# Kernel optimization log

Measured on AMD Instinct MI355X. Metric: run time of the kernel, lower is better.

## Reference

```python
import jax, jax.numpy as jnp
import numpy as np

G = 512        # graphs in batch
N_PER = 256    # nodes per graph (equal-size graphs)
D = 128        # embed_dim
E_PER = 4096   # edges per graph
KEEP = 0.5
K = int(np.ceil(KEEP * N_PER))  # 128 nodes kept per graph (PyG topk: ceil(ratio*n))
N = G * N_PER
E = G * E_PER


def setup_inputs() -> dict:
    key = jax.random.key(0)
    k1, k2, k3, k4, k5 = jax.random.split(key, 5)
    x = jax.random.normal(k1, (N, D), jnp.float32)
    offs = (jnp.arange(G, dtype=jnp.int32) * N_PER)[:, None]
    src = jax.random.randint(k2, (G, E_PER), 0, N_PER, dtype=jnp.int32) + offs
    dst = jax.random.randint(k3, (G, E_PER), 0, N_PER, dtype=jnp.int32) + offs
    edge_index = jnp.stack([src.reshape(-1), dst.reshape(-1)], axis=0)  # [2, E], within-graph edges
    graph_indicator = jnp.repeat(jnp.arange(G, dtype=jnp.int32), N_PER)  # [N]
    gcn_w = jax.random.normal(k4, (D, 1), jnp.float32) / np.sqrt(D)
    gcn_b = jnp.zeros((1,), jnp.float32)
    lin_w = jax.random.normal(k5, (2 * D, D), jnp.float32) / np.sqrt(2 * D)
    lin_b = jnp.zeros((D,), jnp.float32)
    return {"input_feature": x, "graph_indicator": graph_indicator, "edge_index": edge_index,
            "gcn_w": gcn_w, "gcn_b": gcn_b, "lin_w": lin_w, "lin_b": lin_b}


def gcn_conv(x, edge_index, w, b):
    # PyG GCNConv: add self-loops, symmetric normalization, aggregate at target (edge_index[1]).
    n = x.shape[0]
    loop = jnp.arange(n, dtype=edge_index.dtype)
    row = jnp.concatenate([edge_index[0], loop])  # source
    col = jnp.concatenate([edge_index[1], loop])  # target
    deg = jax.ops.segment_sum(jnp.ones_like(col, dtype=x.dtype), col, num_segments=n)
    dinv = jax.lax.rsqrt(deg)  # deg >= 1 due to self-loops
    norm = dinv[row] * dinv[col]            # [E+N]
    xw = x @ w                              # [N, out]
    msg = xw[row] * norm[:, None]           # gather + scale
    agg = jax.ops.segment_sum(msg, col, num_segments=n)
    return agg + b


def reference(input_feature, graph_indicator, edge_index, gcn_w, gcn_b, lin_w, lin_b):
    # SAGPool: attention scores via GCNConv(d -> 1)
    score = gcn_conv(input_feature, edge_index, gcn_w, gcn_b).squeeze(-1)  # [N]
    # per-graph top-k mask (equal-size graphs -> reshape)
    s = score.reshape(G, N_PER)
    _, idx = jax.lax.top_k(s, K)                                          # [G, K]
    mask = jnp.zeros((G, N_PER), bool).at[jnp.arange(G)[:, None], idx].set(True)
    # gated features of kept nodes: x[mask] * tanh(score[mask])
    feat = (input_feature * jnp.tanh(score)[:, None]).reshape(G, N_PER, D)
    m = mask[..., None]
    # global mean/max pool over kept nodes per graph (exactly K kept per graph)
    mean = jnp.sum(jnp.where(m, feat, 0.0), axis=1) / K                   # [G, D]
    mx = jnp.max(jnp.where(m, feat, -jnp.inf), axis=1)                    # [G, D]
    readout = jnp.concatenate([mean, mx], axis=1)                         # [G, 2D]
    return readout @ lin_w + lin_b                                        # [G, D]
```

## Files before the change

### kernel.cpp

```cpp
#include <hip/hip_runtime.h>
#include <math.h>

#define NG   512
#define NPER 256
#define DD   128
#define EPER 4096
#define KK   128
#define NT   1024
#define NW   16

__global__ __launch_bounds__(NT, 4) void sag_fused(
    const float* __restrict__ x,
    const int*   __restrict__ esrc,
    const int*   __restrict__ edst,
    const float* __restrict__ gcn_w,
    const float* __restrict__ gcn_b,
    const float* __restrict__ lin_w,
    const float* __restrict__ lin_b,
    float* __restrict__ out)
{
  const int g    = blockIdx.x;
  const int tid  = threadIdx.x;
  const int lane = tid & 63;
  const int wave = tid >> 6;

  __shared__ float  sXW[NPER];
  __shared__ float  sScore[NPER];
  __shared__ float  sDinv[NPER];
  __shared__ int    sDeg[NPER];
  __shared__ int    sRank[NPER];
  __shared__ int    sKept[KK];
  __shared__ float  sGateK[KK];
  __shared__ float2 sPS[NW][64];
  __shared__ float2 sPM[NW][64];
  __shared__ float2 sR2[DD];

  const int4* es4 = (const int4*)(esrc + (size_t)g * EPER);
  const int4* ed4 = (const int4*)(edst + (size_t)g * EPER);
  int4 ev_s = es4[tid];
  int4 ev_d = ed4[tid];

  if (tid < NPER) { sDeg[tid] = 1; sRank[tid] = 0; }
  __syncthreads();

  const float*  xg  = x + (size_t)g * NPER * DD;
  const float4* xg4 = (const float4*)xg;
  const int sl   = lane & 31;
  const int half = lane >> 5;
  float4 wr4 = ((const float4*)gcn_w)[sl];
  #pragma unroll
  for (int r = 0; r < 8; ++r) {
    int node = r * 32 + wave * 2 + half;
    float4 q = xg4[node * 32 + sl];
    float acc = q.x*wr4.x + q.y*wr4.y + q.z*wr4.z + q.w*wr4.w;
    acc += __shfl_xor(acc, 1);
    acc += __shfl_xor(acc, 2);
    acc += __shfl_xor(acc, 4);
    acc += __shfl_xor(acc, 8);
    acc += __shfl_xor(acc, 16);
    if (sl == 0) sXW[node] = acc;
  }

  atomicAdd(&sDeg[ev_d.x & 255], 1);
  atomicAdd(&sDeg[ev_d.y & 255], 1);
  atomicAdd(&sDeg[ev_d.z & 255], 1);
  atomicAdd(&sDeg[ev_d.w & 255], 1);
  __syncthreads();

  if (tid < NPER) {
    float dv = 1.0f / sqrtf((float)sDeg[tid]);
    sDinv[tid]  = dv;
    sScore[tid] = sXW[tid] * dv * dv;
  }
  __syncthreads();

  {
    int s0 = ev_s.x & 255, d0 = ev_d.x & 255;
    int s1 = ev_s.y & 255, d1 = ev_d.y & 255;
    int s2 = ev_s.z & 255, d2 = ev_d.z & 255;
    int s3 = ev_s.w & 255, d3 = ev_d.w & 255;
    atomicAdd(&sScore[d0], sXW[s0] * sDinv[s0] * sDinv[d0]);
    atomicAdd(&sScore[d1], sXW[s1] * sDinv[s1] * sDinv[d1]);
    atomicAdd(&sScore[d2], sXW[s2] * sDinv[s2] * sDinv[d2]);
    atomicAdd(&sScore[d3], sXW[s3] * sDinv[s3] * sDinv[d3]);
  }
  __syncthreads();

  {
    int node = tid & 255;
    int seg  = tid >> 8;
    float s_i = sScore[node];
    int base = seg * 64;
    int part = 0;
    #pragma unroll 8
    for (int jj = base; jj < base + 64; ++jj) {
      float s_j = sScore[jj];
      part += (s_j > s_i) || (s_j == s_i && jj < node);
    }
    atomicAdd(&sRank[node], part);
  }
  __syncthreads();
  {
    const float bval = gcn_b[0];
    if (tid < NPER) {
      int r = sRank[tid];
      if (r < KK) {
        sKept[r]  = tid;
        sGateK[r] = tanhf(sScore[tid] + bval);
      }
    }
  }
  __syncthreads();

  const float2* xg2 = (const float2*)xg;
  float sm0 = 0.f, sm1 = 0.f, mx0 = -INFINITY, mx1 = -INFINITY;
  #pragma unroll
  for (int t = 0; t < 8; ++t) {
    int kidx = wave * 8 + t;
    int node = sKept[kidx];
    float gt = sGateK[kidx];
    float2 p = xg2[node * 64 + lane];
    float a = p.x * gt, b = p.y * gt;
    sm0 += a; sm1 += b;
    mx0 = fmaxf(mx0, a); mx1 = fmaxf(mx1, b);
  }
  sPS[wave][lane] = make_float2(sm0, sm1);
  sPM[wave][lane] = make_float2(mx0, mx1);
  __syncthreads();

  if (wave == 0) {
    float2 a = sPS[0][lane];
    #pragma unroll
    for (int w = 1; w < NW; ++w) { float2 p = sPS[w][lane]; a.x += p.x; a.y += p.y; }
    sR2[lane] = make_float2(a.x * (1.0f / KK), a.y * (1.0f / KK));
  } else if (wave == 1) {
    float2 a = sPM[0][lane];
    #pragma unroll
    for (int w = 1; w < NW; ++w) {
      float2 p = sPM[w][lane];
      a.x = fmaxf(a.x, p.x); a.y = fmaxf(a.y, p.y);
    }
    sR2[64 + lane] = a;
  }
  __syncthreads();

  const float*  sR  = (const float*)sR2;
  const float2* lw2 = (const float2*)lin_w;
  float a0 = 0.f, a1 = 0.f;
  #pragma unroll
  for (int t = 0; t < 16; ++t) {
    int k = wave * 16 + t;
    float rv = sR[k];
    float2 p = lw2[k * 64 + lane];
    a0 += rv * p.x;
    a1 += rv * p.y;
  }
  __syncthreads();
  sPS[wave][lane] = make_float2(a0, a1);
  __syncthreads();
  if (wave == 0) {
    float2 a = sPS[0][lane];
    #pragma unroll
    for (int w = 1; w < NW; ++w) { float2 p = sPS[w][lane]; a.x += p.x; a.y += p.y; }
    float2 bb = ((const float2*)lin_b)[lane];
    a.x += bb.x; a.y += bb.y;
    ((float2*)out)[(size_t)g * 64 + lane] = a;
  }
}

extern "C" void kernel_launch(void* const* d_in, const int* in_sizes, int n_in,
                              void* d_out, int out_size, void* d_ws, size_t ws_size,
                              hipStream_t stream) {
  const float* x  = (const float*)d_in[0];
  const int*   ei = (const int*)d_in[2];
  const float* gw = (const float*)d_in[3];
  const float* gb = (const float*)d_in[4];
  const float* lw = (const float*)d_in[5];
  const float* lb = (const float*)d_in[6];
  float* out = (float*)d_out;
  const int E = in_sizes[2] / 2;
  sag_fused<<<NG, NT, 0, stream>>>(x, ei, ei + E, gw, gb, lw, lb, out);
}
```

Before: 138.2 us.

## Halve block size and give each thread more vectorised work per stage

```diff
diff --git a/kernel.cpp b/kernel.cpp
--- a/kernel.cpp
+++ b/kernel.cpp
@@ -6,8 +6,8 @@
 #define DD   128
 #define EPER 4096
 #define KK   128
-#define NT   1024
-#define NW   16
+#define NT   512
+#define NW   8
 
 __global__ __launch_bounds__(NT, 4) void sag_fused(
     const float* __restrict__ x,
@@ -25,64 +25,80 @@
   const int wave = tid >> 6;
 
   __shared__ float  sXW[NPER];
-  __shared__ float  sScore[NPER];
+  __shared__ float  sXWn[NPER];
   __shared__ float  sDinv[NPER];
   __shared__ int    sDeg[NPER];
   __shared__ int    sRank[NPER];
-  __shared__ int    sKept[KK];
-  __shared__ float  sGateK[KK];
+  __shared__ float4 sScore4[NPER / 4];
+  __shared__ int2   sKG[KK];
   __shared__ float2 sPS[NW][64];
   __shared__ float2 sPM[NW][64];
   __shared__ float2 sR2[DD];
+  float* sScore = (float*)sScore4;
 
   const int4* es4 = (const int4*)(esrc + (size_t)g * EPER);
   const int4* ed4 = (const int4*)(edst + (size_t)g * EPER);
-  int4 ev_s = es4[tid];
-  int4 ev_d = ed4[tid];
+  int4 sa = es4[tid], sb = es4[NT + tid];
+  int4 da = ed4[tid], db = ed4[NT + tid];
 
   if (tid < NPER) { sDeg[tid] = 1; sRank[tid] = 0; }
   __syncthreads();
 
   const float*  xg  = x + (size_t)g * NPER * DD;
   const float4* xg4 = (const float4*)xg;
-  const int sl   = lane & 31;
-  const int half = lane >> 5;
-  float4 wr4 = ((const float4*)gcn_w)[sl];
+  const int j   = lane & 15;
+  const int sub = lane >> 4;
+  float4 wa = ((const float4*)gcn_w)[j];
+  float4 wb = ((const float4*)gcn_w)[16 + j];
   #pragma unroll
   for (int r = 0; r < 8; ++r) {
-    int node = r * 32 + wave * 2 + half;
-    float4 q = xg4[node * 32 + sl];
-    float acc = q.x*wr4.x + q.y*wr4.y + q.z*wr4.z + q.w*wr4.w;
+    int node = r * 32 + wave * 4 + sub;
+    float4 q0 = xg4[node * 32 + j];
+    float4 q1 = xg4[node * 32 + 16 + j];
+    float acc = q0.x*wa.x + q0.y*wa.y + q0.z*wa.z + q0.w*wa.w
+              + q1.x*wb.x + q1.y*wb.y + q1.z*wb.z + q1.w*wb.w;
     acc += __shfl_xor(acc, 1);
     acc += __shfl_xor(acc, 2);
     acc += __shfl_xor(acc, 4);
     acc += __shfl_xor(acc, 8);
-    acc += __shfl_xor(acc, 16);
-    if (sl == 0) sXW[node] = acc;
+    if (j == 0) sXW[node] = acc;
   }
-
-  atomicAdd(&sDeg[ev_d.x & 255], 1);
-  atomicAdd(&sDeg[ev_d.y & 255], 1);
-  atomicAdd(&sDeg[ev_d.z & 255], 1);
-  atomicAdd(&sDeg[ev_d.w & 255], 1);
+  atomicAdd(&sDeg[da.x & 255], 1);
+  atomicAdd(&sDeg[da.y & 255], 1);
+  atomicAdd(&sDeg[da.z & 255], 1);
+  atomicAdd(&sDeg[da.w & 255], 1);
+  atomicAdd(&sDeg[db.x & 255], 1);
+  atomicAdd(&sDeg[db.y & 255], 1);
+  atomicAdd(&sDeg[db.z & 255], 1);
+  atomicAdd(&sDeg[db.w & 255], 1);
   __syncthreads();
 
   if (tid < NPER) {
-    float dv = 1.0f / sqrtf((float)sDeg[tid]);
+    float dv  = 1.0f / sqrtf((float)sDeg[tid]);
+    float xwn = sXW[tid] * dv;
     sDinv[tid]  = dv;
-    sScore[tid] = sXW[tid] * dv * dv;
+    sXWn[tid]   = xwn;
+    sScore[tid] = xwn * dv;
   }
   __syncthreads();
 
   {
-    int s0 = ev_s.x & 255, d0 = ev_d.x & 255;
-    int s1 = ev_s.y & 255, d1 = ev_d.y & 255;
-    int s2 = ev_s.z & 255, d2 = ev_d.z & 255;
-    int s3 = ev_s.w & 255, d3 = ev_d.w & 255;
-    atomicAdd(&sScore[d0], sXW[s0] * sDinv[s0] * sDinv[d0]);
-    atomicAdd(&sScore[d1], sXW[s1] * sDinv[s1] * sDinv[d1]);
-    atomicAdd(&sScore[d2], sXW[s2] * sDinv[s2] * sDinv[d2]);
-    atomicAdd(&sScore[d3], sXW[s3] * sDinv[s3] * sDinv[d3]);
+    int s0 = sa.x & 255, d0 = da.x & 255;
+    int s1 = sa.y & 255, d1 = da.y & 255;
+    int s2 = sa.z & 255, d2 = da.z & 255;
+    int s3 = sa.w & 255, d3 = da.w & 255;
+    int s4 = sb.x & 255, d4 = db.x & 255;
+    int s5 = sb.y & 255, d5 = db.y & 255;
+    int s6 = sb.z & 255, d6 = db.z & 255;
+    int s7 = sb.w & 255, d7 = db.w & 255;
+    atomicAdd(&sScore[d0], sXWn[s0] * sDinv[d0]);
+    atomicAdd(&sScore[d1], sXWn[s1] * sDinv[d1]);
+    atomicAdd(&sScore[d2], sXWn[s2] * sDinv[d2]);
+    atomicAdd(&sScore[d3], sXWn[s3] * sDinv[d3]);
+    atomicAdd(&sScore[d4], sXWn[s4] * sDinv[d4]);
+    atomicAdd(&sScore[d5], sXWn[s5] * sDinv[d5]);
+    atomicAdd(&sScore[d6], sXWn[s6] * sDinv[d6]);
+    atomicAdd(&sScore[d7], sXWn[s7] * sDinv[d7]);
   }
   __syncthreads();
 
@@ -90,12 +106,16 @@
     int node = tid & 255;
     int seg  = tid >> 8;
     float s_i = sScore[node];
-    int base = seg * 64;
+    int base = seg * 32;
     int part = 0;
     #pragma unroll 8
-    for (int jj = base; jj < base + 64; ++jj) {
-      float s_j = sScore[jj];
-      part += (s_j > s_i) || (s_j == s_i && jj < node);
+    for (int t = 0; t < 32; ++t) {
+      float4 v = sScore4[base + t];
+      int jj = (base + t) * 4;
+      part += (v.x > s_i) || (v.x == s_i && (jj + 0) < node);
+      part += (v.y > s_i) || (v.y == s_i && (jj + 1) < node);
+      part += (v.z > s_i) || (v.z == s_i && (jj + 2) < node);
+      part += (v.w > s_i) || (v.w == s_i && (jj + 3) < node);
     }
     atomicAdd(&sRank[node], part);
   }
@@ -104,10 +124,7 @@
     const float bval = gcn_b[0];
     if (tid < NPER) {
       int r = sRank[tid];
-      if (r < KK) {
-        sKept[r]  = tid;
-        sGateK[r] = tanhf(sScore[tid] + bval);
-      }
+      if (r < KK) sKG[r] = make_int2(tid, __float_as_int(tanhf(sScore[tid] + bval)));
     }
   }
   __syncthreads();
@@ -115,11 +132,10 @@
   const float2* xg2 = (const float2*)xg;
   float sm0 = 0.f, sm1 = 0.f, mx0 = -INFINITY, mx1 = -INFINITY;
   #pragma unroll
-  for (int t = 0; t < 8; ++t) {
-    int kidx = wave * 8 + t;
-    int node = sKept[kidx];
-    float gt = sGateK[kidx];
-    float2 p = xg2[node * 64 + lane];
+  for (int t = 0; t < 16; ++t) {
+    int2 kg = sKG[wave * 16 + t];
+    float gt = __int_as_float(kg.y);
+    float2 p = xg2[kg.x * 64 + lane];
     float a = p.x * gt, b = p.y * gt;
     sm0 += a; sm1 += b;
     mx0 = fmaxf(mx0, a); mx1 = fmaxf(mx1, b);
@@ -127,7 +143,6 @@
   sPS[wave][lane] = make_float2(sm0, sm1);
   sPM[wave][lane] = make_float2(mx0, mx1);
   __syncthreads();
-
   if (wave == 0) {
     float2 a = sPS[0][lane];
     #pragma unroll
@@ -144,18 +159,17 @@
   }
   __syncthreads();
 
-  const float*  sR  = (const float*)sR2;
   const float2* lw2 = (const float2*)lin_w;
   float a0 = 0.f, a1 = 0.f;
   #pragma unroll
   for (int t = 0; t < 16; ++t) {
-    int k = wave * 16 + t;
-    float rv = sR[k];
-    float2 p = lw2[k * 64 + lane];
-    a0 += rv * p.x;
-    a1 += rv * p.y;
+    int k2 = wave * 16 + t;
+    float2 rv = sR2[k2];
+    float2 p0 = lw2[(2 * k2) * 64 + lane];
+    float2 p1 = lw2[(2 * k2 + 1) * 64 + lane];
+    a0 += rv.x * p0.x + rv.y * p1.x;
+    a1 += rv.x * p0.y + rv.y * p1.y;
   }
-  __syncthreads();
   sPS[wave][lane] = make_float2(a0, a1);
   __syncthreads();
   if (wave == 0) {
```

New measurement: 128.8 us. 6.8% less time.
